# Performance work log

Measured on AMD Instinct MI355X. Metric: run time of the kernel, lower is better.

Reference implementation:

```python
import jax, jax.numpy as jnp
import numpy as np

RANK, A1, A2, B1, B2 = 64, 64, 64, 64, 64
N_TOKENS = 8192


def _xavier_uniform(key, shape, fan_in, fan_out, dtype=jnp.float32):
    bound = float(np.sqrt(6.0 / (fan_in + fan_out)))
    return jax.random.uniform(key, shape, dtype, -bound, bound)


def setup_inputs() -> dict:
    key = jax.random.key(0)
    kx, ka, kb, kbias = jax.random.split(key, 4)
    x = jax.random.normal(kx, (N_TOKENS, A1 * B1), dtype=jnp.float32)
    # torch xavier on a 3D tensor (rank, d1, d2): fan_in = d1*d2, fan_out = rank*d2
    a = _xavier_uniform(ka, (RANK, A1, A2), A1 * A2, RANK * A2)
    b = _xavier_uniform(kb, (RANK, B1, B2), B1 * B2, RANK * B2)
    bias = jax.random.normal(kbias, (A2 * B2,), dtype=jnp.float32)
    return {"x": x, "a": a, "b": b, "bias": bias}


def reference(x, a, b, bias):
    r, a1, a2 = a.shape
    _, b1, b2 = b.shape
    # w = sum_r kron(a_r, b_r):  w[i*b1+k, j*b2+l] = sum_r a[r,i,j] * b[r,k,l]
    w = jnp.einsum('rij,rkl->ikjl', a, b).reshape(a1 * b1, a2 * b2)
    out = x @ w  # (N, a2*b2)
    return out + bias[None, :]
```

## Files before the change

kernel.cpp:

```cpp
#include <hip/hip_runtime.h>
#include <hip/hip_bf16.h>


#define M_DIM 8192
#define N_DIM 4096
#define K_DIM 4096
#define KT_COUNT 128
#define NPACK 512

typedef __attribute__((ext_vector_type(8))) short short8;
typedef __attribute__((ext_vector_type(4))) float floatx4;

typedef __attribute__((address_space(1))) void gvoid_t;
typedef __attribute__((address_space(3))) void lvoid_t;

static __device__ __forceinline__ void gl_lds16(const void* g, const void* l) {
  __builtin_amdgcn_global_load_lds((gvoid_t*)(unsigned long long)g,
                                   (lvoid_t*)(unsigned int)(unsigned long long)l,
                                   16, 0, 0);
}

static __device__ __forceinline__ unsigned short f2bf(float f) {
  unsigned int u = __builtin_bit_cast(unsigned int, f);
  u = (u + 0x7fffu + ((u >> 16) & 1u)) >> 16;
  return (unsigned short)u;
}

__global__ __launch_bounds__(512) void prep_kernel(
    const float* __restrict__ x, const float* __restrict__ a,
    const float* __restrict__ b, unsigned short* __restrict__ Xp,
    unsigned short* __restrict__ Wp) {
  __shared__ float lds_a[1024];
  const int bid = blockIdx.x;
  const int t = threadIdx.x;

  if (bid < NPACK) {
    const int M0 = bid >> 3;
    const int mm0 = (bid & 7) * 16;
    const int kt = t >> 2, c = t & 3;
    const float* src = x + (size_t)(M0 * 128 + mm0) * K_DIM + t * 8;
    unsigned short* dst =
        Xp + (size_t)(M0 * KT_COUNT + kt) * 4096 + (mm0 * 4 + c) * 8;
#pragma unroll 4
    for (int r = 0; r < 16; ++r) {
      float4 v0 = ((const float4*)src)[0];
      float4 v1 = ((const float4*)src)[1];
      short8 o;
      o[0] = (short)f2bf(v0.x); o[1] = (short)f2bf(v0.y);
      o[2] = (short)f2bf(v0.z); o[3] = (short)f2bf(v0.w);
      o[4] = (short)f2bf(v1.x); o[5] = (short)f2bf(v1.y);
      o[6] = (short)f2bf(v1.z); o[7] = (short)f2bf(v1.w);
      *(short8*)dst = o;
      src += K_DIM;
      dst += 32;
    }
  } else {
    const int bw = bid - NPACK;
    const int rg = bw & 255;
    const int i = rg >> 2;
    const int j0 = (rg & 3) * 16;
    const int k0 = (bw >> 8) * 8;

    if (t < 256) {
      const int r = t >> 2, jq = t & 3;
      float4 v = ((const float4*)(a + (size_t)r * 4096 + i * 64 + j0))[jq];
      ((float4*)lds_a)[r * 4 + jq] = v;
    }
    __syncthreads();

    if (t < 256) {
      const int l = t & 63;
      const int jj = t >> 6;
      float acc[4][8];
#pragma unroll
      for (int jp = 0; jp < 4; ++jp)
#pragma unroll
        for (int kb = 0; kb < 8; ++kb) acc[jp][kb] = 0.f;

      const float* bb = b + k0 * 64 + l;
#pragma unroll 4
      for (int r = 0; r < 64; ++r) {
        float4 aj = ((const float4*)lds_a)[r * 4 + jj];
        float bv[8];
#pragma unroll
        for (int kb = 0; kb < 8; ++kb) bv[kb] = bb[(size_t)r * 4096 + kb * 64];
        const float av[4] = {aj.x, aj.y, aj.z, aj.w};
#pragma unroll
        for (int jp = 0; jp < 4; ++jp)
#pragma unroll
          for (int kb = 0; kb < 8; ++kb)
            acc[jp][kb] = fmaf(av[jp], bv[kb], acc[jp][kb]);
      }

      const int kt = (i * 64 + k0) >> 5;
      const int c = (k0 & 31) >> 3;
#pragma unroll
      for (int jp = 0; jp < 4; ++jp) {
        const int j = j0 + jj * 4 + jp;
        const int n = j * 64 + l;
        const int blob = (n >> 7) * KT_COUNT + kt;
        const int pos = c * 128 + (n & 127);
        short8 o;
#pragma unroll
        for (int kb = 0; kb < 8; ++kb) o[kb] = (short)f2bf(acc[jp][kb]);
        *(short8*)(Wp + (size_t)blob * 4096 + pos * 8) = o;
      }
    }
  }
}

#define BAR() asm volatile("s_barrier" ::: "memory")
#define WAIT_VM(N) asm volatile("s_waitcnt vmcnt(" #N ")" ::: "memory")
#define WAIT_LGKM0() asm volatile("s_waitcnt lgkmcnt(0)" ::: "memory")

__global__ __launch_bounds__(512, 2) void gemm_kernel(
    const unsigned short* __restrict__ Xp, const unsigned short* __restrict__ Wp,
    const float* __restrict__ bias, float* __restrict__ out) {
  __shared__ short8 As[4][2][512];
  __shared__ short8 Bs[4][2][512];

  const int bid = blockIdx.x;
  const int xcd = bid & 7;
  const int pos = bid >> 3;
  const int N0 = xcd * 2 + (pos & 1);
  const int M0 = pos >> 1;

  const int t = threadIdx.x;
  const int wave = t >> 6, lane = t & 63;
  const int l16 = lane & 15, quad = lane >> 4;
  const int wm = wave & 1;
  const int wn = wave >> 1;

  floatx4 acc[8][4];
#pragma unroll
  for (int mt = 0; mt < 8; ++mt)
#pragma unroll
    for (int nt = 0; nt < 4; ++nt) acc[mt][nt] = (floatx4){0.f, 0.f, 0.f, 0.f};

  const int pt = ((t & 127) << 2) | (t >> 7);
  const unsigned short* gA0 = Xp + (size_t)(M0 * 2 + 0) * KT_COUNT * 4096 + (size_t)pt * 8;
  const unsigned short* gA1 = Xp + (size_t)(M0 * 2 + 1) * KT_COUNT * 4096 + (size_t)pt * 8;
  const unsigned short* gB0 = Wp + (size_t)(N0 * 2 + 0) * KT_COUNT * 4096 + (size_t)t * 8;
  const unsigned short* gB1 = Wp + (size_t)(N0 * 2 + 1) * KT_COUNT * 4096 + (size_t)t * 8;

#pragma unroll
  for (int s = 0; s < 3; ++s) {
    gl_lds16(gA0 + (size_t)s * 4096, &As[s][0][t]);
    gl_lds16(gA1 + (size_t)s * 4096, &As[s][1][t]);
    gl_lds16(gB0 + (size_t)s * 4096, &Bs[s][0][t]);
    gl_lds16(gB1 + (size_t)s * 4096, &Bs[s][1][t]);
  }
  WAIT_VM(8);
  BAR();

  const int ra = quad * 128 + l16;
  const int rb = quad * 128 + (wn & 1) * 64 + l16;
  const int bh = wn >> 1;

#pragma unroll 2
  for (int kt = 0; kt < KT_COUNT; ++kt) {
    const int tb = kt & 3;
    const int db = (kt + 3) & 3;
    const size_t soff =
        (size_t)((kt + 3 < KT_COUNT) ? kt + 3 : KT_COUNT - 1) * 4096;

    short8 bf[4], af[4];

#pragma unroll
    for (int nt = 0; nt < 4; ++nt) bf[nt] = Bs[tb][bh][rb + nt * 16];
#pragma unroll
    for (int m = 0; m < 4; ++m) af[m] = As[tb][wm][ra + m * 16];
    gl_lds16(gA0 + soff, &As[db][0][t]);
    gl_lds16(gA1 + soff, &As[db][1][t]);
    BAR();
    WAIT_LGKM0();
    __builtin_amdgcn_sched_barrier(0);
    __builtin_amdgcn_s_setprio(1);
#pragma unroll
    for (int m = 0; m < 4; ++m)
#pragma unroll
      for (int nt = 0; nt < 4; ++nt)
        acc[m][nt] = __builtin_amdgcn_mfma_f32_16x16x32_bf16(
            af[m], bf[nt], acc[m][nt], 0, 0, 0);
    __builtin_amdgcn_s_setprio(0);
    __builtin_amdgcn_sched_barrier(0);
    BAR();

#pragma unroll
    for (int m = 0; m < 4; ++m) af[m] = As[tb][wm][ra + (4 + m) * 16];
    gl_lds16(gB0 + soff, &Bs[db][0][t]);
    gl_lds16(gB1 + soff, &Bs[db][1][t]);
    WAIT_VM(8);
    BAR();
    WAIT_LGKM0();
    __builtin_amdgcn_sched_barrier(0);
    __builtin_amdgcn_s_setprio(1);
#pragma unroll
    for (int m = 0; m < 4; ++m)
#pragma unroll
      for (int nt = 0; nt < 4; ++nt)
        acc[4 + m][nt] = __builtin_amdgcn_mfma_f32_16x16x32_bf16(
            af[m], bf[nt], acc[4 + m][nt], 0, 0, 0);
    __builtin_amdgcn_s_setprio(0);
    __builtin_amdgcn_sched_barrier(0);
    BAR();
  }

  const int col_base = N0 * 256 + wn * 64;
  const int row_base = M0 * 256 + wm * 128;
#pragma unroll
  for (int nt = 0; nt < 4; ++nt) {
    const int col = col_base + nt * 16 + l16;
    const float bv = bias[col];
#pragma unroll
    for (int mt = 0; mt < 8; ++mt) {
      floatx4 v = acc[mt][nt];
#pragma unroll
      for (int r4 = 0; r4 < 4; ++r4) {
        const int row = row_base + mt * 16 + quad * 4 + r4;
        out[(size_t)row * N_DIM + col] = v[r4] + bv;
      }
    }
  }
}

extern "C" void kernel_launch(void* const* d_in, const int* in_sizes, int n_in,
                              void* d_out, int out_size, void* d_ws, size_t ws_size,
                              hipStream_t stream) {
  const float* x = (const float*)d_in[0];
  const float* a = (const float*)d_in[1];
  const float* b = (const float*)d_in[2];
  const float* bias = (const float*)d_in[3];
  float* out = (float*)d_out;

  unsigned short* Xp = (unsigned short*)d_ws;
  unsigned short* Wp = Xp + (size_t)M_DIM * K_DIM;

  prep_kernel<<<NPACK + 2048, 512, 0, stream>>>(x, a, b, Xp, Wp);
  gemm_kernel<<<512, 512, 0, stream>>>(Xp, Wp, bias, out);
}
```

Before: 487.1 us.

## Transpose X pack through swizzled LDS and reorder prep blocks

The X pack blocks now stage a 128-row by 256-column tile through XOR-swizzled shared memory, so the packed Xp blob is written in the same c-major order that Wp uses. This lets the GEMM load A with a plain thread-linear index instead of a permuted one. The W-build blocks are moved ahead of the pack blocks in the grid, and the pack grid doubles to 1024 blocks. The aim is more coalesced, contiguous global writes in prep and simpler A addressing in the GEMM, at the cost of a 64KB LDS staging buffer and an extra barrier.

```diff
diff --git a/kernel.cpp b/kernel.cpp
--- a/kernel.cpp
+++ b/kernel.cpp
@@ -6,7 +6,8 @@
 #define N_DIM 4096
 #define K_DIM 4096
 #define KT_COUNT 128
-#define NPACK 512
+#define NBUILD 2048
+#define NPACK 1024
 
 typedef __attribute__((ext_vector_type(8))) short short8;
 typedef __attribute__((ext_vector_type(4))) float floatx4;
@@ -30,19 +31,74 @@
     const float* __restrict__ x, const float* __restrict__ a,
     const float* __restrict__ b, unsigned short* __restrict__ Xp,
     unsigned short* __restrict__ Wp) {
-  __shared__ float lds_a[1024];
+  __shared__ short8 smem[4096];
   const int bid = blockIdx.x;
   const int t = threadIdx.x;
 
-  if (bid < NPACK) {
-    const int M0 = bid >> 3;
-    const int mm0 = (bid & 7) * 16;
-    const int kt = t >> 2, c = t & 3;
-    const float* src = x + (size_t)(M0 * 128 + mm0) * K_DIM + t * 8;
-    unsigned short* dst =
-        Xp + (size_t)(M0 * KT_COUNT + kt) * 4096 + (mm0 * 4 + c) * 8;
+  if (bid < NBUILD) {
+    float* lds_a = (float*)smem;
+    const int rg = bid & 255;
+    const int i = rg >> 2;
+    const int j0 = (rg & 3) * 16;
+    const int k0 = (bid >> 8) * 8;
+
+    if (t < 256) {
+      const int r = t >> 2, jq = t & 3;
+      float4 v = ((const float4*)(a + (size_t)r * 4096 + i * 64 + j0))[jq];
+      ((float4*)lds_a)[r * 4 + jq] = v;
+    }
+    __syncthreads();
+
+    if (t < 256) {
+      const int l = t & 63;
+      const int jj = t >> 6;
+      float acc[4][8];
+#pragma unroll
+      for (int jp = 0; jp < 4; ++jp)
+#pragma unroll
+        for (int kb = 0; kb < 8; ++kb) acc[jp][kb] = 0.f;
+
+      const float* bb = b + k0 * 64 + l;
 #pragma unroll 4
-    for (int r = 0; r < 16; ++r) {
+      for (int r = 0; r < 64; ++r) {
+        float4 aj = ((const float4*)lds_a)[r * 4 + jj];
+        float bv[8];
+#pragma unroll
+        for (int kb = 0; kb < 8; ++kb) bv[kb] = bb[(size_t)r * 4096 + kb * 64];
+        const float av[4] = {aj.x, aj.y, aj.z, aj.w};
+#pragma unroll
+        for (int jp = 0; jp < 4; ++jp)
+#pragma unroll
+          for (int kb = 0; kb < 8; ++kb)
+            acc[jp][kb] = fmaf(av[jp], bv[kb], acc[jp][kb]);
+      }
+
+      const int kt = (i * 64 + k0) >> 5;
+      const int c = (k0 & 31) >> 3;
+#pragma unroll
+      for (int jp = 0; jp < 4; ++jp) {
+        const int j = j0 + jj * 4 + jp;
+        const int n = j * 64 + l;
+        const int blob = (n >> 7) * KT_COUNT + kt;
+        const int pos = c * 128 + (n & 127);
+        short8 o;
+#pragma unroll
+        for (int kb = 0; kb < 8; ++kb) o[kb] = (short)f2bf(acc[jp][kb]);
+        *(short8*)(Wp + (size_t)blob * 4096 + pos * 8) = o;
+      }
+    }
+  } else {
+    const int pid = bid - NBUILD;
+    const int M0 = pid >> 4;
+    const int kg = pid & 15;
+    const int rsub = t >> 5;
+    const int col8 = t & 31;
+
+#pragma unroll
+    for (int p = 0; p < 8; ++p) {
+      const int row = p * 16 + rsub;
+      const float* src =
+          x + (size_t)(M0 * 128 + row) * K_DIM + kg * 256 + col8 * 8;
       float4 v0 = ((const float4*)src)[0];
       float4 v1 = ((const float4*)src)[1];
       short8 o;
@@ -50,61 +106,17 @@
       o[2] = (short)f2bf(v0.z); o[3] = (short)f2bf(v0.w);
       o[4] = (short)f2bf(v1.x); o[5] = (short)f2bf(v1.y);
       o[6] = (short)f2bf(v1.z); o[7] = (short)f2bf(v1.w);
-      *(short8*)dst = o;
-      src += K_DIM;
-      dst += 32;
-    }
-  } else {
-    const int bw = bid - NPACK;
-    const int rg = bw & 255;
-    const int i = rg >> 2;
-    const int j0 = (rg & 3) * 16;
-    const int k0 = (bw >> 8) * 8;
-
-    if (t < 256) {
-      const int r = t >> 2, jq = t & 3;
-      float4 v = ((const float4*)(a + (size_t)r * 4096 + i * 64 + j0))[jq];
-      ((float4*)lds_a)[r * 4 + jq] = v;
+      smem[row * 32 + (col8 ^ (row & 31))] = o;
     }
     __syncthreads();
 
-    if (t < 256) {
-      const int l = t & 63;
-      const int jj = t >> 6;
-      float acc[4][8];
-#pragma unroll
-      for (int jp = 0; jp < 4; ++jp)
-#pragma unroll
-        for (int kb = 0; kb < 8; ++kb) acc[jp][kb] = 0.f;
-
-      const float* bb = b + k0 * 64 + l;
-#pragma unroll 4
-      for (int r = 0; r < 64; ++r) {
-        float4 aj = ((const float4*)lds_a)[r * 4 + jj];
-        float bv[8];
-#pragma unroll
-        for (int kb = 0; kb < 8; ++kb) bv[kb] = bb[(size_t)r * 4096 + kb * 64];
-        const float av[4] = {aj.x, aj.y, aj.z, aj.w};
-#pragma unroll
-        for (int jp = 0; jp < 4; ++jp)
-#pragma unroll
-          for (int kb = 0; kb < 8; ++kb)
-            acc[jp][kb] = fmaf(av[jp], bv[kb], acc[jp][kb]);
-      }
-
-      const int kt = (i * 64 + k0) >> 5;
-      const int c = (k0 & 31) >> 3;
-#pragma unroll
-      for (int jp = 0; jp < 4; ++jp) {
-        const int j = j0 + jj * 4 + jp;
-        const int n = j * 64 + l;
-        const int blob = (n >> 7) * KT_COUNT + kt;
-        const int pos = c * 128 + (n & 127);
-        short8 o;
-#pragma unroll
-        for (int kb = 0; kb < 8; ++kb) o[kb] = (short)f2bf(acc[jp][kb]);
-        *(short8*)(Wp + (size_t)blob * 4096 + pos * 8) = o;
-      }
+    const int c = t >> 7, mm = t & 127;
+    unsigned short* dst =
+        Xp + (size_t)(M0 * KT_COUNT + kg * 8) * 4096 + t * 8;
+#pragma unroll
+    for (int q = 0; q < 8; ++q) {
+      short8 v = smem[mm * 32 + ((q * 4 + c) ^ (mm & 31))];
+      *(short8*)(dst + (size_t)q * 4096) = v;
     }
   }
 }
@@ -137,9 +149,8 @@
 #pragma unroll
     for (int nt = 0; nt < 4; ++nt) acc[mt][nt] = (floatx4){0.f, 0.f, 0.f, 0.f};
 
-  const int pt = ((t & 127) << 2) | (t >> 7);
-  const unsigned short* gA0 = Xp + (size_t)(M0 * 2 + 0) * KT_COUNT * 4096 + (size_t)pt * 8;
-  const unsigned short* gA1 = Xp + (size_t)(M0 * 2 + 1) * KT_COUNT * 4096 + (size_t)pt * 8;
+  const unsigned short* gA0 = Xp + (size_t)(M0 * 2 + 0) * KT_COUNT * 4096 + (size_t)t * 8;
+  const unsigned short* gA1 = Xp + (size_t)(M0 * 2 + 1) * KT_COUNT * 4096 + (size_t)t * 8;
   const unsigned short* gB0 = Wp + (size_t)(N0 * 2 + 0) * KT_COUNT * 4096 + (size_t)t * 8;
   const unsigned short* gB1 = Wp + (size_t)(N0 * 2 + 1) * KT_COUNT * 4096 + (size_t)t * 8;
 
@@ -236,6 +247,6 @@
   unsigned short* Xp = (unsigned short*)d_ws;
   unsigned short* Wp = Xp + (size_t)M_DIM * K_DIM;
 
-  prep_kernel<<<NPACK + 2048, 512, 0, stream>>>(x, a, b, Xp, Wp);
+  prep_kernel<<<NBUILD + NPACK, 512, 0, stream>>>(x, a, b, Xp, Wp);
   gemm_kernel<<<512, 512, 0, stream>>>(Xp, Wp, bias, out);
 }
```

Result: slower. 502.2 us (+3.1%).
